# Kernel optimization log

Hardware: AMD Instinct MI355X
Metric: run time of the kernel (lower is better)

## Reference

```python
import jax, jax.numpy as jnp
import numpy as np

T, N, E, H = 10, 2048, 32768, 256
EPS = 1e-12  # F.normalize eps
COORDS_WEIGHT = 1.0


def setup_inputs() -> dict:
    key = jax.random.key(0)
    ks = jax.random.split(key, 16)

    def lin_w(k, fan_in, fan_out, gain=1.0):
        return (jax.random.normal(k, (fan_in, fan_out), jnp.float32)
                * gain / np.sqrt(fan_in)).astype(jnp.float32)

    return {
        "x": jax.random.normal(ks[0], (T, N, 4, 3), jnp.float32),
        "h": jax.random.normal(ks[1], (T, N, H), jnp.float32),
        "others": jax.random.normal(ks[2], (T, N, H), jnp.float32),
        # edge_mlp: Linear(2H+16 -> H), ReLU, Linear(H -> H), ReLU
        "We1": lin_w(ks[3], 2 * H + 16, H), "be1": jnp.zeros((H,), jnp.float32),
        "We2": lin_w(ks[4], H, H), "be2": jnp.zeros((H,), jnp.float32),
        # node_mlp: Linear(H + H + H -> H), ReLU, Linear(H -> H)
        "Wn1": lin_w(ks[5], 3 * H, H), "bn1": jnp.zeros((H,), jnp.float32),
        "Wn2": lin_w(ks[6], H, H), "bn2": jnp.zeros((H,), jnp.float32),
        # coord_mlp: Linear(H -> H), ReLU, Linear(H -> 1, bias=False, xavier gain 0.001)
        "Wc1": lin_w(ks[7], H, H), "bc1": jnp.zeros((H,), jnp.float32),
        "Wc2": lin_w(ks[8], H, 1, gain=0.001),
        "edge_index": jax.random.randint(ks[9], (2, E), 0, N, jnp.int64),
    }


def reference(x, h, others, We1, be1, We2, be2, Wn1, bn1, Wn2, bn2,
              Wc1, bc1, Wc2, edge_index):
    row, col = edge_index[0], edge_index[1]
    n_nodes = x.shape[1]

    # coord2radial (vectorized over the per-timestep python loop)
    coord_diff = x[:, row] - x[:, col]                      # [T,E,4,3]
    gram = jnp.einsum('tejd,tekd->tejk', coord_diff, coord_diff)
    gram = gram.reshape(gram.shape[0], gram.shape[1], 16)   # [T,E,16]
    radial = gram / jnp.maximum(
        jnp.linalg.norm(gram, axis=-1, keepdims=True), EPS)

    # edge_model: cat([source, target, radial]) -> MLP
    edge_in = jnp.concatenate([h[:, row], h[:, col], radial], axis=-1)
    e = jax.nn.relu(edge_in @ We1 + be1)
    e = jax.nn.relu(e @ We2 + be2)                          # [T,E,H]

    # coord_model: trans = coord_diff * coord_mlp(edge_feat)
    m = jax.nn.relu(e @ Wc1 + bc1) @ Wc2                    # [T,E,1]
    trans = coord_diff * m[..., None]                       # [T,E,4,3]

    seg_sum = lambda a: jax.vmap(
        lambda v: jax.ops.segment_sum(v, row, num_segments=n_nodes))(a)
    counts = jax.ops.segment_sum(
        jnp.ones((row.shape[0],), x.dtype), row, num_segments=n_nodes)
    counts = jnp.maximum(counts, 1.0)

    f = (seg_sum(trans) / counts[None, :, None, None]) * COORDS_WEIGHT
    coord_out = x + f                                       # [T,N,4,3]

    # node_model: agg = segment_sum(edge_feat, row); cat([others, h, agg])
    agg = seg_sum(e)                                        # [T,N,H]
    node_in = jnp.concatenate([others, h, agg], axis=-1)    # [T,N,3H]
    n_out = jax.nn.relu(node_in @ Wn1 + bn1) @ Wn2 + bn2
    h_out = h + n_out                                       # recurrent residual
    return h_out, coord_out
```

## Files before the change

kernel.cpp:

```cpp
#include <hip/hip_runtime.h>
#include <hip/hip_bf16.h>
#include <stdint.h>

#define TT 10
#define NN 2048
#define EE 32768
#define HH 256

typedef short bf16x8 __attribute__((ext_vector_type(8)));
typedef float f32x4 __attribute__((ext_vector_type(4)));

__device__ __forceinline__ float b2f(unsigned short u) {
    unsigned int x = ((unsigned int)u) << 16;
    return __builtin_bit_cast(float, x);
}
__device__ __forceinline__ unsigned short f2b(float f) {
    unsigned int x = __builtin_bit_cast(unsigned int, f);
    unsigned int r = x + 0x7FFFu + ((x >> 16) & 1u);
    return (unsigned short)(r >> 16);
}

#define GLOAD_LDS16(g, l)                                                      \
    __builtin_amdgcn_global_load_lds(                                          \
        (const __attribute__((address_space(1))) void*)(g),                    \
        (__attribute__((address_space(3))) void*)(l), 16, 0, 0)


__global__ void cvt_bf16_kernel(const float* __restrict__ in,
                                unsigned short* __restrict__ out, int n) {
    int i = blockIdx.x * blockDim.x + threadIdx.x;
    int stride = gridDim.x * blockDim.x;
    for (; i < n; i += stride) out[i] = f2b(in[i]);
}

__global__ void transpose_all_kernel(
    const float* __restrict__ We1, const float* __restrict__ We2,
    const float* __restrict__ Wn1, const float* __restrict__ Wn2,
    const float* __restrict__ Wc1,
    unsigned short* __restrict__ We1at, unsigned short* __restrict__ We1bt,
    unsigned short* __restrict__ Wrt, unsigned short* __restrict__ We2t,
    unsigned short* __restrict__ Wn1t, unsigned short* __restrict__ Wn2t,
    unsigned short* __restrict__ Wc1t) {
    int idx = blockIdx.x * blockDim.x + threadIdx.x;
    const int s1 = 65536;
    const int s2 = s1 + 65536;
    const int s3 = s2 + 16384;
    const int s4 = s3 + 65536;
    const int s5 = s4 + 196608;
    const int s6 = s5 + 65536;
    const int s7 = s6 + 65536;
    if (idx >= s7) return;
    if (idx < s1) {
        int li = idx, n = li >> 8, k = li & 255;
        We1at[li] = f2b(We1[k * 256 + n]);
    } else if (idx < s2) {
        int li = idx - s1, n = li >> 8, k = li & 255;
        We1bt[li] = f2b(We1[(256 + k) * 256 + n]);
    } else if (idx < s3) {
        int li = idx - s2, n = li >> 6, k = li & 63;
        Wrt[li] = (k < 16) ? f2b(We1[(512 + k) * 256 + n]) : (unsigned short)0;
    } else if (idx < s4) {
        int li = idx - s3, n = li >> 8, k = li & 255;
        We2t[li] = f2b(We2[k * 256 + n]);
    } else if (idx < s5) {
        int li = idx - s4, n = li / 768, k = li - n * 768;
        Wn1t[li] = f2b(Wn1[k * 256 + n]);
    } else if (idx < s6) {
        int li = idx - s5, n = li >> 8, k = li & 255;
        Wn2t[li] = f2b(Wn2[k * 256 + n]);
    } else {
        int li = idx - s6, n = li >> 8, k = li & 255;
        Wc1t[li] = f2b(Wc1[k * 256 + n]);
    }
}

__global__ void zero_f32_kernel(float* __restrict__ p, int n) {
    int i = blockIdx.x * blockDim.x + threadIdx.x;
    int stride = gridDim.x * blockDim.x;
    for (; i < n; i += stride) p[i] = 0.0f;
}

__global__ void count_kernel(const int* __restrict__ rows, int* __restrict__ counts) {
    int e = blockIdx.x * blockDim.x + threadIdx.x;
    if (e < EE) atomicAdd(&counts[rows[e]], 1);
}

__global__ __launch_bounds__(256) void scan_kernel(const int* __restrict__ counts,
                                                   int* __restrict__ boff) {
    __shared__ int part[256];
    int tid = threadIdx.x;
    int base = tid * 8;
    int local[8];
    int s = 0;
#pragma unroll
    for (int i = 0; i < 8; ++i) { local[i] = s; s += counts[base + i]; }
    part[tid] = s;
    __syncthreads();
    for (int offd = 1; offd < 256; offd <<= 1) {
        int v = (tid >= offd) ? part[tid - offd] : 0;
        __syncthreads();
        part[tid] += v;
        __syncthreads();
    }
    int pbase = (tid == 0) ? 0 : part[tid - 1];
#pragma unroll
    for (int i = 0; i < 8; ++i) boff[base + i] = pbase + local[i];
    if (tid == 255) boff[2048] = pbase + s;
}

__global__ void scatter_kernel(const int* __restrict__ rows, const int* __restrict__ cols,
                               const int* __restrict__ boff, int* __restrict__ cursor,
                               int* __restrict__ rs, int* __restrict__ cs) {
    int e = blockIdx.x * blockDim.x + threadIdx.x;
    if (e < EE) {
        int r = rows[e];
        int pos = boff[r] + atomicAdd(&cursor[r], 1);
        rs[pos] = r;
        cs[pos] = cols[e];
    }
}


__device__ __forceinline__ void stageB(const unsigned short* __restrict__ Wt,
                                       int KPAD, int k0, int tid, int w,
                                       unsigned short* Bs) {
    int trow = tid >> 3;
    int sk8 = ((tid & 7) ^ (trow & 7)) * 8;
#pragma unroll
    for (int i = 0; i < 8; ++i) {
        int row = i * 32 + trow;
        GLOAD_LDS16(Wt + (size_t)row * KPAD + k0 + sk8, Bs + i * 2048 + w * 512);
    }
}

__device__ __forceinline__ void mfma_step(const unsigned short* As,
                                          const unsigned short* Bs,
                                          int w, int lr, int lq, f32x4 acc[4][4]) {
    int xs = (lr & 7) << 3;
#pragma unroll
    for (int kk = 0; kk < 64; kk += 32) {
        bf16x8 a[4], b[4];
        int pc = (kk + lq * 8) ^ xs;
#pragma unroll
        for (int m = 0; m < 4; ++m)
            a[m] = *reinterpret_cast<const bf16x8*>(As + (m * 16 + lr) * 64 + pc);
#pragma unroll
        for (int n = 0; n < 4; ++n)
            b[n] = *reinterpret_cast<const bf16x8*>(
                Bs + (w * 64 + n * 16 + lr) * 64 + pc);
#pragma unroll
        for (int m = 0; m < 4; ++m)
#pragma unroll
            for (int n = 0; n < 4; ++n)
                acc[m][n] = __builtin_amdgcn_mfma_f32_16x16x32_bf16(
                    a[m], b[n], acc[m][n], 0, 0, 0);
    }
}

__device__ __forceinline__ void mfma_step_es(const unsigned short* Es,
                                             const unsigned short* Bs, int k0,
                                             int w, int lr, int lq, f32x4 acc[4][4]) {
    int xs = (lr & 7) << 3;
#pragma unroll
    for (int kk = 0; kk < 64; kk += 32) {
        bf16x8 a[4], b[4];
        int lcol = kk + lq * 8;
#pragma unroll
        for (int m = 0; m < 4; ++m)
            a[m] = *reinterpret_cast<const bf16x8*>(
                Es + (m * 16 + lr) * 256 + ((k0 + lcol) ^ xs));
#pragma unroll
        for (int n = 0; n < 4; ++n)
            b[n] = *reinterpret_cast<const bf16x8*>(
                Bs + (w * 64 + n * 16 + lr) * 64 + (lcol ^ xs));
#pragma unroll
        for (int m = 0; m < 4; ++m)
#pragma unroll
            for (int n = 0; n < 4; ++n)
                acc[m][n] = __builtin_amdgcn_mfma_f32_16x16x32_bf16(
                    a[m], b[n], acc[m][n], 0, 0, 0);
    }
}

__global__ __launch_bounds__(256, 2) void edge_mega_kernel(
    const float* __restrict__ x,
    const float* __restrict__ Ya, const float* __restrict__ Yb,
    const unsigned short* __restrict__ Wrt,
    const unsigned short* __restrict__ We2t, const float* __restrict__ be2,
    const unsigned short* __restrict__ Wc1t, const float* __restrict__ bc1,
    const float* __restrict__ Wc2,
    const int* __restrict__ rs, const int* __restrict__ cs,
    float* __restrict__ aggf, float* __restrict__ csum) {
    __shared__ unsigned short As[64 * 64];
    __shared__ unsigned short Bs[256 * 64];
    __shared__ unsigned short Es[64 * 256];
    __shared__ float CDs[64][12];
    __shared__ unsigned short Rs[64][16];
    __shared__ float Ms[64][4];

    int tid = threadIdx.x;
    int lane = tid & 63, w = tid >> 6;
    int lr = lane & 15, lq = lane >> 4;
    int blockRow = blockIdx.x * 64;
    int tt = blockRow >> 15;
    int sb = blockRow & (EE - 1);

    if (tid < 64) {
        int s = sb + tid;
        int r = rs[s], c = cs[s];
        const float* xr = x + ((size_t)tt * NN + r) * 12;
        const float* xc = x + ((size_t)tt * NN + c) * 12;
        float cd[12];
#pragma unroll
        for (int i = 0; i < 12; ++i) {
            cd[i] = xr[i] - xc[i];
            CDs[tid][i] = cd[i];
        }
        float g[16], ss = 0.f;
#pragma unroll
        for (int j = 0; j < 4; ++j)
#pragma unroll
            for (int k = 0; k < 4; ++k) {
                float v = cd[j * 3] * cd[k * 3] + cd[j * 3 + 1] * cd[k * 3 + 1] +
                          cd[j * 3 + 2] * cd[k * 3 + 2];
                g[j * 4 + k] = v;
                ss += v * v;
            }
        float inv = 1.f / fmaxf(sqrtf(ss), 1e-12f);
#pragma unroll
        for (int i = 0; i < 16; ++i) Rs[tid][i] = f2b(g[i] * inv);
    }

    int trow = tid >> 3;

    __syncthreads();

    f32x4 acc[4][4];
#pragma unroll
    for (int m = 0; m < 4; ++m)
#pragma unroll
        for (int n = 0; n < 4; ++n) acc[m][n] = (f32x4){0.f, 0.f, 0.f, 0.f};

    {
#pragma unroll
        for (int j = 0; j < 2; ++j) {
            int row = j * 32 + trow;
            int lseg = (tid & 7) ^ (row & 7);
            bf16x8 v = {};
            if (lseg < 2) {
#pragma unroll
                for (int ii = 0; ii < 8; ++ii)
                    v[ii] = (short)Rs[row][lseg * 8 + ii];
            }
            *reinterpret_cast<bf16x8*>(As + row * 64 + (tid & 7) * 8) = v;
        }
        stageB(Wrt, 64, 0, tid, w, Bs);
        __syncthreads();
        mfma_step(As, Bs, w, lr, lq, acc);
        __syncthreads();
    }
    {
#pragma unroll
        for (int m = 0; m < 4; ++m)
#pragma unroll
            for (int r = 0; r < 4; ++r) {
                int row = m * 16 + lq * 4 + r;
                int e = sb + row;
                int ar = rs[e], ac = cs[e];
                const float* pa = Ya + ((size_t)tt * NN + ar) * 256;
                const float* pb = Yb + ((size_t)tt * NN + ac) * 256;
                int xsw = (row & 7) << 3;
#pragma unroll
                for (int n = 0; n < 4; ++n) {
                    int col = w * 64 + n * 16 + lr;
                    float v = fmaxf(acc[m][n][r] + pa[col] + pb[col], 0.f);
                    Es[row * 256 + (col ^ xsw)] = f2b(v);
                }
            }
    }
    __syncthreads();

#pragma unroll
    for (int m = 0; m < 4; ++m)
#pragma unroll
        for (int n = 0; n < 4; ++n) acc[m][n] = (f32x4){0.f, 0.f, 0.f, 0.f};
#pragma unroll 1
    for (int k0 = 0; k0 < 256; k0 += 64) {
        stageB(We2t, 256, k0, tid, w, Bs);
        __syncthreads();
        mfma_step_es(Es, Bs, k0, w, lr, lq, acc);
        __syncthreads();
    }
    {
        float bv[4];
#pragma unroll
        for (int n = 0; n < 4; ++n) bv[n] = be2[w * 64 + n * 16 + lr];
#pragma unroll
        for (int m = 0; m < 4; ++m)
#pragma unroll
            for (int r = 0; r < 4; ++r) {
                int row = m * 16 + lq * 4 + r;
                int xsw = (row & 7) << 3;
#pragma unroll
                for (int n = 0; n < 4; ++n) {
                    int col = w * 64 + n * 16 + lr;
                    float v = fmaxf(acc[m][n][r] + bv[n], 0.f);
                    Es[row * 256 + (col ^ xsw)] = f2b(v);
                }
            }
    }
    __syncthreads();

#pragma unroll
    for (int m = 0; m < 4; ++m)
#pragma unroll
        for (int n = 0; n < 4; ++n) acc[m][n] = (f32x4){0.f, 0.f, 0.f, 0.f};
#pragma unroll 1
    for (int k0 = 0; k0 < 256; k0 += 64) {
        stageB(Wc1t, 256, k0, tid, w, Bs);
        __syncthreads();
        mfma_step_es(Es, Bs, k0, w, lr, lq, acc);
        __syncthreads();
    }
    {
        float bv[4], wv[4];
#pragma unroll
        for (int n = 0; n < 4; ++n) {
            int col = w * 64 + n * 16 + lr;
            bv[n] = bc1[col];
            wv[n] = Wc2[col];
        }
#pragma unroll
        for (int m = 0; m < 4; ++m)
#pragma unroll
            for (int r = 0; r < 4; ++r) {
                float p = 0.f;
#pragma unroll
                for (int n = 0; n < 4; ++n)
                    p += fmaxf(acc[m][n][r] + bv[n], 0.f) * wv[n];
                p += __shfl_xor(p, 1);
                p += __shfl_xor(p, 2);
                p += __shfl_xor(p, 4);
                p += __shfl_xor(p, 8);
                if (lr == 0) Ms[m * 16 + lq * 4 + r][w] = p;
            }
    }
    __syncthreads();

    if (tid < 64) {
        Ms[tid][0] = Ms[tid][0] + Ms[tid][1] + Ms[tid][2] + Ms[tid][3];
    }
    __syncthreads();

    {
        float accv = 0.f;
        for (int i = 0; i < 64; ++i) {
            int ncur = rs[sb + i];
            accv += b2f(Es[i * 256 + (tid ^ ((i & 7) << 3))]);
            if (i == 63 || rs[sb + i + 1] != ncur) {
                atomicAdd(&aggf[((size_t)tt * NN + ncur) * 256 + tid], accv);
                accv = 0.f;
            }
        }
    }
    if (tid < 12) {
        float a = 0.f;
        for (int i = 0; i < 64; ++i) {
            int ncur = rs[sb + i];
            a += CDs[i][tid] * Ms[i][0];
            if (i == 63 || rs[sb + i + 1] != ncur) {
                atomicAdd(&csum[((size_t)tt * NN + ncur) * 12 + tid], a);
                a = 0.f;
            }
        }
    }
}

template<int EPI>
__global__ __launch_bounds__(256) void gemm_kernel(
    const unsigned short* __restrict__ A, const unsigned short* __restrict__ Wt,
    const float* __restrict__ bias, unsigned short* __restrict__ Cb, int KPAD,
    const float* __restrict__ resid, float* __restrict__ outf) {
    __shared__ unsigned short As[128 * 32];
    __shared__ unsigned short Bs[128 * 32];
    int tid = threadIdx.x;
    int lane = tid & 63, w = tid >> 6;
    int wr = w >> 1, wc = w & 1;
    int blockRow = blockIdx.x * 128, colBase = blockIdx.y * 128;
    int l4 = lane >> 2;
    int seg = lane & 3;

    int ar0 = blockRow + w * 16 + l4;
    int br0 = colBase + w * 16 + l4;
    const unsigned short* pA0 = A + (size_t)ar0 * KPAD + seg * 8;
    const unsigned short* pA1 = pA0 + (size_t)64 * KPAD;
    const unsigned short* pB0 = Wt + (size_t)br0 * KPAD + seg * 8;
    const unsigned short* pB1 = pB0 + (size_t)64 * KPAD;

    unsigned short* ldsA = As + w * 512;
    unsigned short* ldsB = Bs + w * 512;

    f32x4 acc[4][4] = {};
    int lr = lane & 15, lq = lane >> 4;

    for (int k0 = 0; k0 < KPAD; k0 += 32) {
        GLOAD_LDS16(pA0 + k0, ldsA);
        GLOAD_LDS16(pA1 + k0, ldsA + 2048);
        GLOAD_LDS16(pB0 + k0, ldsB);
        GLOAD_LDS16(pB1 + k0, ldsB + 2048);
        __syncthreads();
        bf16x8 a[4], b[4];
#pragma unroll
        for (int m = 0; m < 4; ++m)
            a[m] = *reinterpret_cast<const bf16x8*>(
                As + (wr * 64 + m * 16 + lr) * 32 + lq * 8);
#pragma unroll
        for (int n = 0; n < 4; ++n)
            b[n] = *reinterpret_cast<const bf16x8*>(
                Bs + (wc * 64 + n * 16 + lr) * 32 + lq * 8);
#pragma unroll
        for (int m = 0; m < 4; ++m)
#pragma unroll
            for (int n = 0; n < 4; ++n)
                acc[m][n] = __builtin_amdgcn_mfma_f32_16x16x32_bf16(
                    a[m], b[n], acc[m][n], 0, 0, 0);
        __syncthreads();
    }

    float bv[4];
#pragma unroll
    for (int n = 0; n < 4; ++n) bv[n] = bias[colBase + wc * 64 + n * 16 + lr];

#pragma unroll
    for (int m = 0; m < 4; ++m)
#pragma unroll
        for (int r = 0; r < 4; ++r) {
            int row = blockRow + wr * 64 + m * 16 + lq * 4 + r;
#pragma unroll
            for (int n = 0; n < 4; ++n) {
                int col = colBase + wc * 64 + n * 16 + lr;
                float v = acc[m][n][r] + bv[n];
                if (EPI == 2) {
                    outf[(size_t)row * 256 + col] =
                        v + resid[(size_t)row * 256 + col];
                } else if (EPI == 1) {
                    outf[(size_t)row * 256 + col] = v;
                } else {
                    Cb[(size_t)row * 256 + col] = f2b(fmaxf(v, 0.f));
                }
            }
        }
}

__global__ void nodein_kernel(const float* __restrict__ others,
                              const unsigned short* __restrict__ hb,
                              const float* __restrict__ aggf,
                              unsigned short* __restrict__ node_in) {
    int idx = blockIdx.x * blockDim.x + threadIdx.x;
    int stride = gridDim.x * blockDim.x;
    const int total = TT * NN * 192;
    for (; idx < total; idx += stride) {
        int nf = idx / 192, c4 = (idx - nf * 192) * 4;
        ushort4 v;
        if (c4 < 256) {
            float4 o = *reinterpret_cast<const float4*>(others + (size_t)nf * 256 + c4);
            v.x = f2b(o.x); v.y = f2b(o.y); v.z = f2b(o.z); v.w = f2b(o.w);
        } else if (c4 < 512) {
            v = *reinterpret_cast<const ushort4*>(hb + (size_t)nf * 256 + (c4 - 256));
        } else {
            float4 a = *reinterpret_cast<const float4*>(aggf + (size_t)nf * 256 + (c4 - 512));
            v.x = f2b(a.x); v.y = f2b(a.y); v.z = f2b(a.z); v.w = f2b(a.w);
        }
        *reinterpret_cast<ushort4*>(node_in + (size_t)nf * 768 + c4) = v;
    }
}

__global__ void coordout_kernel(const float* __restrict__ x, const int* __restrict__ counts,
                                const float* __restrict__ csum, float* __restrict__ outc) {
    int idx = blockIdx.x * blockDim.x + threadIdx.x;
    if (idx >= TT * NN * 12) return;
    int n = (idx / 12) & (NN - 1);
    float cnt = (float)(counts[n] > 0 ? counts[n] : 1);
    outc[idx] = x[idx] + csum[idx] / cnt;
}


extern "C" void kernel_launch(void* const* d_in, const int* in_sizes, int n_in,
                              void* d_out, int out_size, void* d_ws, size_t ws_size,
                              hipStream_t stream) {
    const float* x = (const float*)d_in[0];
    const float* h = (const float*)d_in[1];
    const float* others = (const float*)d_in[2];
    const float* We1 = (const float*)d_in[3];
    const float* be1 = (const float*)d_in[4];
    const float* We2 = (const float*)d_in[5];
    const float* be2 = (const float*)d_in[6];
    const float* Wn1 = (const float*)d_in[7];
    const float* bn1 = (const float*)d_in[8];
    const float* Wn2 = (const float*)d_in[9];
    const float* bn2 = (const float*)d_in[10];
    const float* Wc1 = (const float*)d_in[11];
    const float* bc1 = (const float*)d_in[12];
    const float* Wc2 = (const float*)d_in[13];
    const int* ei = (const int*)d_in[14];
    const int* rows = ei;
    const int* cols = ei + EE;

    char* wsb = (char*)d_ws;
    size_t off = 0;
    auto alloc = [&](size_t bytes) {
        void* p = wsb + off;
        off = (off + bytes + 255) & ~(size_t)255;
        return p;
    };
    const int TNH = TT * NN * HH;
    unsigned short* hb = (unsigned short*)alloc((size_t)TNH * 2);
    unsigned short* We1at = (unsigned short*)alloc(256 * 256 * 2);
    unsigned short* We1bt = (unsigned short*)alloc(256 * 256 * 2);
    unsigned short* Wrt = (unsigned short*)alloc(256 * 64 * 2);
    unsigned short* We2t = (unsigned short*)alloc(256 * 256 * 2);
    unsigned short* Wn1t = (unsigned short*)alloc(256 * 768 * 2);
    unsigned short* Wn2t = (unsigned short*)alloc(256 * 256 * 2);
    unsigned short* Wc1t = (unsigned short*)alloc(256 * 256 * 2);
    float* Ya = (float*)alloc((size_t)TNH * 4);
    float* Yb = (float*)alloc((size_t)TNH * 4);
    float* aggf = (float*)alloc((size_t)TT * NN * 256 * 4);
    float* csum = (float*)alloc((size_t)TT * NN * 12 * 4);
    int* counts = (int*)alloc((size_t)2048 * 4);
    int* cursor = (int*)alloc((size_t)2048 * 4);
    float* zeros256 = (float*)alloc((size_t)256 * 4);
    int* boff = (int*)alloc((size_t)2049 * 4);
    int* rs = (int*)alloc((size_t)EE * 4);
    int* cs = (int*)alloc((size_t)EE * 4);
    unsigned short* node_in = (unsigned short*)alloc((size_t)TT * NN * 768 * 2);
    unsigned short* Z = (unsigned short*)alloc((size_t)TT * NN * 256 * 2);
    (void)ws_size;

    cvt_bf16_kernel<<<2048, 256, 0, stream>>>(h, hb, TNH);
    transpose_all_kernel<<<2112, 256, 0, stream>>>(
        We1, We2, Wn1, Wn2, Wc1, We1at, We1bt, Wrt, We2t, Wn1t, Wn2t, Wc1t);
    zero_f32_kernel<<<17, 256, 0, stream>>>((float*)counts, 4096 + 256);
    count_kernel<<<EE / 256, 256, 0, stream>>>(rows, counts);
    scan_kernel<<<1, 256, 0, stream>>>(counts, boff);
    scatter_kernel<<<EE / 256, 256, 0, stream>>>(rows, cols, boff, cursor, rs, cs);
    zero_f32_kernel<<<2048, 256, 0, stream>>>(aggf, TT * NN * 256 + TT * NN * 12);

    float* houtf = (float*)d_out;
    float* coutf = (float*)d_out + (size_t)TT * NN * HH;

    gemm_kernel<1><<<dim3(TT * NN / 128, 2), 256, 0, stream>>>(
        hb, We1at, be1, nullptr, 256, nullptr, Ya);
    gemm_kernel<1><<<dim3(TT * NN / 128, 2), 256, 0, stream>>>(
        hb, We1bt, zeros256, nullptr, 256, nullptr, Yb);

    edge_mega_kernel<<<TT * EE / 64, 256, 0, stream>>>(
        x, Ya, Yb, Wrt, We2t, be2, Wc1t, bc1, Wc2, rs, cs, aggf, csum);

    nodein_kernel<<<2048, 256, 0, stream>>>(others, hb, aggf, node_in);
    gemm_kernel<0><<<dim3(TT * NN / 128, 2), 256, 0, stream>>>(
        node_in, Wn1t, bn1, Z, 768, nullptr, nullptr);
    gemm_kernel<2><<<dim3(TT * NN / 128, 2), 256, 0, stream>>>(
        Z, Wn2t, bn2, nullptr, 256, h, houtf);

    coordout_kernel<<<(TT * NN * 12 + 255) / 256, 256, 0, stream>>>(
        x, counts, csum, coutf);
}
```

Baseline: 358.7 us.

## Merge node-side edge projections into one bf16 GEMM and slim radial stage

```diff
diff --git a/kernel.cpp b/kernel.cpp
--- a/kernel.cpp
+++ b/kernel.cpp
@@ -36,41 +36,43 @@
 __global__ void transpose_all_kernel(
     const float* __restrict__ We1, const float* __restrict__ We2,
     const float* __restrict__ Wn1, const float* __restrict__ Wn2,
-    const float* __restrict__ Wc1,
-    unsigned short* __restrict__ We1at, unsigned short* __restrict__ We1bt,
-    unsigned short* __restrict__ Wrt, unsigned short* __restrict__ We2t,
-    unsigned short* __restrict__ Wn1t, unsigned short* __restrict__ Wn2t,
-    unsigned short* __restrict__ Wc1t) {
+    const float* __restrict__ Wc1, const float* __restrict__ be1,
+    unsigned short* __restrict__ Wabt, unsigned short* __restrict__ Wrt,
+    unsigned short* __restrict__ We2t, unsigned short* __restrict__ Wn1t,
+    unsigned short* __restrict__ Wn2t, unsigned short* __restrict__ Wc1t,
+    float* __restrict__ bias512) {
     int idx = blockIdx.x * blockDim.x + threadIdx.x;
-    const int s1 = 65536;
-    const int s2 = s1 + 65536;
-    const int s3 = s2 + 16384;
-    const int s4 = s3 + 65536;
-    const int s5 = s4 + 196608;
+    const int s1 = 131072;
+    const int s2 = s1 + 8192;
+    const int s3 = s2 + 65536;
+    const int s4 = s3 + 196608;
+    const int s5 = s4 + 65536;
     const int s6 = s5 + 65536;
-    const int s7 = s6 + 65536;
+    const int s7 = s6 + 512;
     if (idx >= s7) return;
     if (idx < s1) {
         int li = idx, n = li >> 8, k = li & 255;
-        We1at[li] = f2b(We1[k * 256 + n]);
+        int krow = (n < 256) ? k : (256 + k);
+        int col = n & 255;
+        Wabt[li] = f2b(We1[krow * 256 + col]);
     } else if (idx < s2) {
-        int li = idx - s1, n = li >> 8, k = li & 255;
-        We1bt[li] = f2b(We1[(256 + k) * 256 + n]);
+        int li = idx - s1, n = li >> 5, k = li & 31;
+        Wrt[li] = (k < 16) ? f2b(We1[(512 + k) * 256 + n]) : (unsigned short)0;
     } else if (idx < s3) {
-        int li = idx - s2, n = li >> 6, k = li & 63;
-        Wrt[li] = (k < 16) ? f2b(We1[(512 + k) * 256 + n]) : (unsigned short)0;
+        int li = idx - s2, n = li >> 8, k = li & 255;
+        We2t[li] = f2b(We2[k * 256 + n]);
     } else if (idx < s4) {
-        int li = idx - s3, n = li >> 8, k = li & 255;
-        We2t[li] = f2b(We2[k * 256 + n]);
+        int li = idx - s3, n = li / 768, k = li - n * 768;
+        Wn1t[li] = f2b(Wn1[k * 256 + n]);
     } else if (idx < s5) {
-        int li = idx - s4, n = li / 768, k = li - n * 768;
-        Wn1t[li] = f2b(Wn1[k * 256 + n]);
+        int li = idx - s4, n = li >> 8, k = li & 255;
+        Wn2t[li] = f2b(Wn2[k * 256 + n]);
     } else if (idx < s6) {
         int li = idx - s5, n = li >> 8, k = li & 255;
-        Wn2t[li] = f2b(Wn2[k * 256 + n]);
+        Wc1t[li] = f2b(Wc1[k * 256 + n]);
     } else {
-        int li = idx - s6, n = li >> 8, k = li & 255;
-        Wc1t[li] = f2b(Wc1[k * 256 + n]);
+        int li = idx - s6;
+        bias512[li] = (li < 256) ? be1[li] : 0.0f;
     }
 }
 
@@ -121,39 +123,15 @@
 }
 
 
-__device__ __forceinline__ void stageB(const unsigned short* __restrict__ Wt,
-                                       int KPAD, int k0, int tid, int w,
-                                       unsigned short* Bs) {
+__device__ __forceinline__ void stageB64(const unsigned short* __restrict__ Wt,
+                                         int KPAD, int k0, int tid, int w,
+                                         unsigned short* Bs) {
     int trow = tid >> 3;
     int sk8 = ((tid & 7) ^ (trow & 7)) * 8;
 #pragma unroll
     for (int i = 0; i < 8; ++i) {
         int row = i * 32 + trow;
         GLOAD_LDS16(Wt + (size_t)row * KPAD + k0 + sk8, Bs + i * 2048 + w * 512);
-    }
-}
-
-__device__ __forceinline__ void mfma_step(const unsigned short* As,
-                                          const unsigned short* Bs,
-                                          int w, int lr, int lq, f32x4 acc[4][4]) {
-    int xs = (lr & 7) << 3;
-#pragma unroll
-    for (int kk = 0; kk < 64; kk += 32) {
-        bf16x8 a[4], b[4];
-        int pc = (kk + lq * 8) ^ xs;
-#pragma unroll
-        for (int m = 0; m < 4; ++m)
-            a[m] = *reinterpret_cast<const bf16x8*>(As + (m * 16 + lr) * 64 + pc);
-#pragma unroll
-        for (int n = 0; n < 4; ++n)
-            b[n] = *reinterpret_cast<const bf16x8*>(
-                Bs + (w * 64 + n * 16 + lr) * 64 + pc);
-#pragma unroll
-        for (int m = 0; m < 4; ++m)
-#pragma unroll
-            for (int n = 0; n < 4; ++n)
-                acc[m][n] = __builtin_amdgcn_mfma_f32_16x16x32_bf16(
-                    a[m], b[n], acc[m][n], 0, 0, 0);
     }
 }
 
@@ -183,15 +161,14 @@
 }
 
 __global__ __launch_bounds__(256, 2) void edge_mega_kernel(
-    const float* __restrict__ x,
-    const float* __restrict__ Ya, const float* __restrict__ Yb,
+    const float* __restrict__ x, const unsigned short* __restrict__ yab,
     const unsigned short* __restrict__ Wrt,
     const unsigned short* __restrict__ We2t, const float* __restrict__ be2,
     const unsigned short* __restrict__ Wc1t, const float* __restrict__ bc1,
     const float* __restrict__ Wc2,
     const int* __restrict__ rs, const int* __restrict__ cs,
     float* __restrict__ aggf, float* __restrict__ csum) {
-    __shared__ unsigned short As[64 * 64];
+    __shared__ unsigned short As[64 * 32];
     __shared__ unsigned short Bs[256 * 64];
     __shared__ unsigned short Es[64 * 256];
     __shared__ float CDs[64][12];
@@ -205,33 +182,35 @@
     int tt = blockRow >> 15;
     int sb = blockRow & (EE - 1);
 
-    if (tid < 64) {
-        int s = sb + tid;
+    {
+        int el = tid >> 2, j = tid & 3;
+        int s = sb + el;
         int r = rs[s], c = cs[s];
         const float* xr = x + ((size_t)tt * NN + r) * 12;
         const float* xc = x + ((size_t)tt * NN + c) * 12;
         float cd[12];
 #pragma unroll
-        for (int i = 0; i < 12; ++i) {
-            cd[i] = xr[i] - xc[i];
-            CDs[tid][i] = cd[i];
-        }
-        float g[16], ss = 0.f;
-#pragma unroll
-        for (int j = 0; j < 4; ++j)
-#pragma unroll
-            for (int k = 0; k < 4; ++k) {
-                float v = cd[j * 3] * cd[k * 3] + cd[j * 3 + 1] * cd[k * 3 + 1] +
-                          cd[j * 3 + 2] * cd[k * 3 + 2];
-                g[j * 4 + k] = v;
-                ss += v * v;
-            }
+        for (int i = 0; i < 12; ++i) cd[i] = xr[i] - xc[i];
+#pragma unroll
+        for (int d = 0; d < 3; ++d) CDs[el][j * 3 + d] = cd[j * 3 + d];
+        float g4[4], ss = 0.f;
+#pragma unroll
+        for (int k = 0; k < 4; ++k) {
+            float v = cd[j * 3] * cd[k * 3] + cd[j * 3 + 1] * cd[k * 3 + 1] +
+                      cd[j * 3 + 2] * cd[k * 3 + 2];
+            g4[k] = v;
+            ss += v * v;
+        }
+        ss += __shfl_xor(ss, 1);
+        ss += __shfl_xor(ss, 2);
         float inv = 1.f / fmaxf(sqrtf(ss), 1e-12f);
 #pragma unroll
-        for (int i = 0; i < 16; ++i) Rs[tid][i] = f2b(g[i] * inv);
-    }
-
-    int trow = tid >> 3;
+        for (int k = 0; k < 4; ++k) Rs[el][j * 4 + k] = f2b(g4[k] * inv);
+    }
+
+    int srow = tid >> 2, sslot = tid & 3;
+    int xoff32 = (sslot ^ ((srow >> 1) & 3)) * 8;
+    int axoff = (lq ^ ((lr >> 1) & 3)) * 8;
 
     __syncthreads();
 
@@ -242,21 +221,33 @@
         for (int n = 0; n < 4; ++n) acc[m][n] = (f32x4){0.f, 0.f, 0.f, 0.f};
 
     {
-#pragma unroll
-        for (int j = 0; j < 2; ++j) {
-            int row = j * 32 + trow;
-            int lseg = (tid & 7) ^ (row & 7);
-            bf16x8 v = {};
-            if (lseg < 2) {
-#pragma unroll
-                for (int ii = 0; ii < 8; ++ii)
-                    v[ii] = (short)Rs[row][lseg * 8 + ii];
-            }
-            *reinterpret_cast<bf16x8*>(As + row * 64 + (tid & 7) * 8) = v;
-        }
-        stageB(Wrt, 64, 0, tid, w, Bs);
-        __syncthreads();
-        mfma_step(As, Bs, w, lr, lq, acc);
+        int ls = sslot ^ ((srow >> 1) & 3);
+        bf16x8 v = {};
+        if (ls < 2) {
+#pragma unroll
+            for (int ii = 0; ii < 8; ++ii) v[ii] = (short)Rs[srow][ls * 8 + ii];
+        }
+        *reinterpret_cast<bf16x8*>(As + tid * 8) = v;
+#pragma unroll
+        for (int i = 0; i < 4; ++i)
+            GLOAD_LDS16(Wrt + (size_t)(i * 64 + srow) * 32 + xoff32,
+                        Bs + i * 2048 + w * 512);
+        __syncthreads();
+        bf16x8 a[4], b[4];
+#pragma unroll
+        for (int m = 0; m < 4; ++m)
+            a[m] = *reinterpret_cast<const bf16x8*>(
+                As + (m * 16 + lr) * 32 + axoff);
+#pragma unroll
+        for (int n = 0; n < 4; ++n)
+            b[n] = *reinterpret_cast<const bf16x8*>(
+                Bs + (w * 64 + n * 16 + lr) * 32 + axoff);
+#pragma unroll
+        for (int m = 0; m < 4; ++m)
+#pragma unroll
+            for (int n = 0; n < 4; ++n)
+                acc[m][n] = __builtin_amdgcn_mfma_f32_16x16x32_bf16(
+                    a[m], b[n], acc[m][n], 0, 0, 0);
         __syncthreads();
     }
     {
@@ -266,14 +257,13 @@
             for (int r = 0; r < 4; ++r) {
                 int row = m * 16 + lq * 4 + r;
                 int e = sb + row;
-                int ar = rs[e], ac = cs[e];
-                const float* pa = Ya + ((size_t)tt * NN + ar) * 256;
-                const float* pb = Yb + ((size_t)tt * NN + ac) * 256;
+                const unsigned short* pa = yab + ((size_t)tt * NN + rs[e]) * 512;
+                const unsigned short* pb = yab + ((size_t)tt * NN + cs[e]) * 512 + 256;
                 int xsw = (row & 7) << 3;
 #pragma unroll
                 for (int n = 0; n < 4; ++n) {
                     int col = w * 64 + n * 16 + lr;
-                    float v = fmaxf(acc[m][n][r] + pa[col] + pb[col], 0.f);
+                    float v = fmaxf(acc[m][n][r] + b2f(pa[col]) + b2f(pb[col]), 0.f);
                     Es[row * 256 + (col ^ xsw)] = f2b(v);
                 }
             }
@@ -286,7 +276,7 @@
         for (int n = 0; n < 4; ++n) acc[m][n] = (f32x4){0.f, 0.f, 0.f, 0.f};
 #pragma unroll 1
     for (int k0 = 0; k0 < 256; k0 += 64) {
-        stageB(We2t, 256, k0, tid, w, Bs);
+        stageB64(We2t, 256, k0, tid, w, Bs);
         __syncthreads();
         mfma_step_es(Es, Bs, k0, w, lr, lq, acc);
         __syncthreads();
@@ -317,7 +307,7 @@
         for (int n = 0; n < 4; ++n) acc[m][n] = (f32x4){0.f, 0.f, 0.f, 0.f};
 #pragma unroll 1
     for (int k0 = 0; k0 < 256; k0 += 64) {
-        stageB(Wc1t, 256, k0, tid, w, Bs);
+        stageB64(Wc1t, 256, k0, tid, w, Bs);
         __syncthreads();
         mfma_step_es(Es, Bs, k0, w, lr, lq, acc);
         __syncthreads();
@@ -443,8 +433,8 @@
                 if (EPI == 2) {
                     outf[(size_t)row * 256 + col] =
                         v + resid[(size_t)row * 256 + col];
-                } else if (EPI == 1) {
-                    outf[(size_t)row * 256 + col] = v;
+                } else if (EPI == 3) {
+                    Cb[(size_t)row * 512 + col] = f2b(v);
                 } else {
                     Cb[(size_t)row * 256 + col] = f2b(fmaxf(v, 0.f));
                 }
@@ -515,20 +505,18 @@
     };
     const int TNH = TT * NN * HH;
     unsigned short* hb = (unsigned short*)alloc((size_t)TNH * 2);
-    unsigned short* We1at = (unsigned short*)alloc(256 * 256 * 2);
-    unsigned short* We1bt = (unsigned short*)alloc(256 * 256 * 2);
-    unsigned short* Wrt = (unsigned short*)alloc(256 * 64 * 2);
+    unsigned short* Wabt = (unsigned short*)alloc(512 * 256 * 2);
+    unsigned short* Wrt = (unsigned short*)alloc(256 * 32 * 2);
     unsigned short* We2t = (unsigned short*)alloc(256 * 256 * 2);
     unsigned short* Wn1t = (unsigned short*)alloc(256 * 768 * 2);
     unsigned short* Wn2t = (unsigned short*)alloc(256 * 256 * 2);
     unsigned short* Wc1t = (unsigned short*)alloc(256 * 256 * 2);
-    float* Ya = (float*)alloc((size_t)TNH * 4);
-    float* Yb = (float*)alloc((size_t)TNH * 4);
+    float* bias512 = (float*)alloc(512 * 4);
+    unsigned short* yab = (unsigned short*)alloc((size_t)TT * NN * 512 * 2);
     float* aggf = (float*)alloc((size_t)TT * NN * 256 * 4);
     float* csum = (float*)alloc((size_t)TT * NN * 12 * 4);
     int* counts = (int*)alloc((size_t)2048 * 4);
     int* cursor = (int*)alloc((size_t)2048 * 4);
-    float* zeros256 = (float*)alloc((size_t)256 * 4);
     int* boff = (int*)alloc((size_t)2049 * 4);
     int* rs = (int*)alloc((size_t)EE * 4);
     int* cs = (int*)alloc((size_t)EE * 4);
@@ -537,9 +525,9 @@
     (void)ws_size;
 
     cvt_bf16_kernel<<<2048, 256, 0, stream>>>(h, hb, TNH);
-    transpose_all_kernel<<<2112, 256, 0, stream>>>(
-        We1, We2, Wn1, Wn2, Wc1, We1at, We1bt, Wrt, We2t, Wn1t, Wn2t, Wc1t);
-    zero_f32_kernel<<<17, 256, 0, stream>>>((float*)counts, 4096 + 256);
+    transpose_all_kernel<<<2082, 256, 0, stream>>>(
+        We1, We2, Wn1, Wn2, Wc1, be1, Wabt, Wrt, We2t, Wn1t, Wn2t, Wc1t, bias512);
+    zero_f32_kernel<<<16, 256, 0, stream>>>((float*)counts, 4096);
     count_kernel<<<EE / 256, 256, 0, stream>>>(rows, counts);
     scan_kernel<<<1, 256, 0, stream>>>(counts, boff);
     scatter_kernel<<<EE / 256, 256, 0, stream>>>(rows, cols, boff, cursor, rs, cs);
@@ -548,13 +536,11 @@
     float* houtf = (float*)d_out;
     float* coutf = (float*)d_out + (size_t)TT * NN * HH;
 
-    gemm_kernel<1><<<dim3(TT * NN / 128, 2), 256, 0, stream>>>(
-        hb, We1at, be1, nullptr, 256, nullptr, Ya);
-    gemm_kernel<1><<<dim3(TT * NN / 128, 2), 256, 0, stream>>>(
-        hb, We1bt, zeros256, nullptr, 256, nullptr, Yb);
+    gemm_kernel<3><<<dim3(TT * NN / 128, 4), 256, 0, stream>>>(
+        hb, Wabt, bias512, yab, 256, nullptr, nullptr);
 
     edge_mega_kernel<<<TT * EE / 64, 256, 0, stream>>>(
-        x, Ya, Yb, Wrt, We2t, be2, Wc1t, bc1, Wc2, rs, cs, aggf, csum);
+        x, yab, Wrt, We2t, be2, Wc1t, bc1, Wc2, rs, cs, aggf, csum);
 
     nodein_kernel<<<2048, 256, 0, stream>>>(others, hb, aggf, node_in);
     gemm_kernel<0><<<dim3(TT * NN / 128, 2), 256, 0, stream>>>(
```

After: 348.3 us. 2.9% less time.
